# Optimization experiments

Measured on AMD Instinct MI355X. Metric: run time of the kernel, lower is better.

Reference implementation:

```python
import jax, jax.numpy as jnp
import numpy as np

R = 16
ALPHA = 16.0
SCALING = ALPHA / R  # = 1.0


def setup_inputs() -> dict:
    key = jax.random.key(0)
    k1, k2, k3 = jax.random.split(key, 3)
    x = jax.random.normal(k1, (4, 4096, 4096), dtype=jnp.float32)
    A = jax.random.normal(k2, (4096, R), dtype=jnp.float32)
    B = jax.random.normal(k3, (R, 4096), dtype=jnp.float32)
    return {"x": x, "A": A, "B": B}


def reference(x, A, B):
    # Faithful to torch: W_delta = A @ B * scaling; out = x @ W_delta
    # (dropout_p=0.0 so dropout is a no-op)
    W_delta = (A @ B) * SCALING  # [in, out]
    return jnp.matmul(x, W_delta)  # [b, s, out]
```

## Files before the change

kernel.cpp:

```cpp
#include <hip/hip_runtime.h>


constexpr int RANK = 16;
constexpr int K = 4096;
constexpr int N = 4096;
constexpr int M = 4 * 4096;
constexpr int KC = 512;
constexpr int NCHUNK = K / KC;

__global__ __launch_bounds__(512) void lora_fused(const float* __restrict__ x,
                                                  const float* __restrict__ A,
                                                  const float* __restrict__ B,
                                                  float* __restrict__ out) {
  const int tid = threadIdx.x;
  const int lane = tid & 63;
  const int w = tid >> 6;
  const int rg = w & 3;
  const int jg = w >> 2;
  const int rbase = blockIdx.x * 16;
  const int r0 = rbase + rg * 4;
  const int m = (lane >> 2) & 3;

  __shared__ float4 As[KC * 4];
  __shared__ float Ts[16][RANK];

  const float4* __restrict__ A4 = reinterpret_cast<const float4*>(A);

  float vals[32];
#pragma unroll
  for (int i = 0; i < 32; ++i) vals[i] = 0.0f;

  for (int c = 0; c < NCHUNK; ++c) {
    __syncthreads();
#pragma unroll
    for (int q = 0; q < 4; ++q) {
      const int n = q * 512 + tid;
      const int k = n >> 2;
      const int s = n & 3;
      const int p = s ^ ((k >> 2) & 3);
      As[k * 4 + p] = A4[(size_t)c * 2048 + n];
    }
    __syncthreads();

#pragma unroll
    for (int kbi = 0; kbi < 8; ++kbi) {
      const int kl = kbi * 64 + lane;
      const size_t kg = (size_t)c * KC + kl;

      float xv[4];
#pragma unroll
      for (int r = 0; r < 4; ++r) xv[r] = x[(size_t)(r0 + r) * K + kg];

      float4 a[2];
#pragma unroll
      for (int ss = 0; ss < 2; ++ss)
        a[ss] = As[kl * 4 + ((2 * jg + ss) ^ m)];

#pragma unroll
      for (int r = 0; r < 4; ++r) {
#pragma unroll
        for (int ss = 0; ss < 2; ++ss) {
          vals[r * 8 + ss * 4 + 0] = fmaf(xv[r], a[ss].x, vals[r * 8 + ss * 4 + 0]);
          vals[r * 8 + ss * 4 + 1] = fmaf(xv[r], a[ss].y, vals[r * 8 + ss * 4 + 1]);
          vals[r * 8 + ss * 4 + 2] = fmaf(xv[r], a[ss].z, vals[r * 8 + ss * 4 + 2]);
          vals[r * 8 + ss * 4 + 3] = fmaf(xv[r], a[ss].w, vals[r * 8 + ss * 4 + 3]);
        }
      }
    }
  }

#define FOLD(AH, LB)                                           \
  {                                                            \
    const bool hi = (lane & (LB)) != 0;                        \
    _Pragma("unroll")                                          \
    for (int i = 0; i < (AH); ++i) {                           \
      const float send = hi ? vals[i] : vals[i + (AH)];        \
      const float keep = hi ? vals[i + (AH)] : vals[i];        \
      vals[i] = keep + __shfl_xor(send, (LB), 64);             \
    }                                                          \
  }
  FOLD(16, 32)
  FOLD(8, 16)
  FOLD(4, 8)
  FOLD(2, 4)
  FOLD(1, 2)
#undef FOLD
  vals[0] += __shfl_xor(vals[0], 1, 64);

  if (!(lane & 1)) {
    const int e = lane >> 1;
    Ts[rg * 4 + (e >> 3)][jg * 8 + (e & 7)] = vals[0];
  }
  __syncthreads();

  const float2* __restrict__ B2 = reinterpret_cast<const float2*>(B);
  float2* __restrict__ out2 = reinterpret_cast<float2*>(out);

#pragma unroll 1
  for (int cc = 0; cc < 4; ++cc) {
    const int col = w * 512 + cc * 128 + lane * 2;

    float2 b[16];
#pragma unroll
    for (int j = 0; j < RANK; ++j) b[j] = B2[((size_t)j * N + col) >> 1];

#pragma unroll 1
    for (int r = 0; r < 16; ++r) {
      const float4* __restrict__ tr4 =
          reinterpret_cast<const float4*>(&Ts[r][0]);
      const float4 t0 = tr4[0];
      const float4 t1 = tr4[1];
      const float4 t2 = tr4[2];
      const float4 t3 = tr4[3];
      const float tsv[16] = {t0.x, t0.y, t0.z, t0.w, t1.x, t1.y, t1.z, t1.w,
                             t2.x, t2.y, t2.z, t2.w, t3.x, t3.y, t3.z, t3.w};

      float2 acc;
      acc.x = acc.y = 0.0f;
#pragma unroll
      for (int j = 0; j < RANK; ++j) {
        acc.x = fmaf(tsv[j], b[j].x, acc.x);
        acc.y = fmaf(tsv[j], b[j].y, acc.y);
      }
      out2[((size_t)(rbase + r) * N + col) >> 1] = acc;
    }
  }
}

extern "C" void kernel_launch(void* const* d_in, const int* in_sizes, int n_in,
                              void* d_out, int out_size, void* d_ws, size_t ws_size,
                              hipStream_t stream) {
  const float* x = (const float*)d_in[0];
  const float* A = (const float*)d_in[1];
  const float* B = (const float*)d_in[2];
  float* out = (float*)d_out;
  (void)d_ws; (void)ws_size;

  lora_fused<<<M / 16, 512, 0, stream>>>(x, A, B, out);
}
```

Before: 138.6 us.

## Process two row tiles per block, overlapping first tile's output with second's reduction

Each block now handles 32 rows in two halves of 16. While it computes x@A for the second half, it interleaves the B-projection and output stores for the first half into the chunk loop. The point is to overlap the write-heavy output phase with the read-heavy x streaming, and to use float4 B loads and out stores. The trade-off is half as many blocks, which lowers parallelism over the 256 CUs and adds register pressure and extra global B loads inside the hot loop.

```diff
diff --git a/kernel.cpp b/kernel.cpp
--- a/kernel.cpp
+++ b/kernel.cpp
@@ -7,6 +7,8 @@
 constexpr int M = 4 * 4096;
 constexpr int KC = 512;
 constexpr int NCHUNK = K / KC;
+constexpr int ROWST = 16;
+constexpr int ROWSB = 32;
 
 __global__ __launch_bounds__(512) void lora_fused(const float* __restrict__ x,
                                                   const float* __restrict__ A,
@@ -17,97 +19,123 @@
   const int w = tid >> 6;
   const int rg = w & 3;
   const int jg = w >> 2;
-  const int rbase = blockIdx.x * 16;
-  const int r0 = rbase + rg * 4;
+  const int rbase = blockIdx.x * ROWSB;
   const int m = (lane >> 2) & 3;
 
   __shared__ float4 As[KC * 4];
-  __shared__ float Ts[16][RANK];
+  __shared__ float Ts[2][ROWST][RANK];
 
   const float4* __restrict__ A4 = reinterpret_cast<const float4*>(A);
+  const float4* __restrict__ B4 = reinterpret_cast<const float4*>(B);
+  float4* __restrict__ out4 = reinterpret_cast<float4*>(out);
 
-  float vals[32];
+  for (int half = 0; half < 2; ++half) {
+    const int r0 = rbase + half * ROWST + rg * 4;
+
+    float vals[32];
 #pragma unroll
-  for (int i = 0; i < 32; ++i) vals[i] = 0.0f;
+    for (int i = 0; i < 32; ++i) vals[i] = 0.0f;
 
-  for (int c = 0; c < NCHUNK; ++c) {
-    __syncthreads();
+    for (int c = 0; c < NCHUNK; ++c) {
+      __syncthreads();
 #pragma unroll
-    for (int q = 0; q < 4; ++q) {
-      const int n = q * 512 + tid;
-      const int k = n >> 2;
-      const int s = n & 3;
-      const int p = s ^ ((k >> 2) & 3);
-      As[k * 4 + p] = A4[(size_t)c * 2048 + n];
-    }
-    __syncthreads();
+      for (int q = 0; q < 4; ++q) {
+        const int n = q * 512 + tid;
+        const int k = n >> 2;
+        const int s = n & 3;
+        const int p = s ^ ((k >> 2) & 3);
+        As[k * 4 + p] = A4[(size_t)c * 2048 + n];
+      }
+      __syncthreads();
+
+      if (half == 1) {
+        const int rr0 = 2 * c, rr1 = 2 * c + 1;
+#pragma unroll 1
+        for (int cc = 0; cc < 2; ++cc) {
+          const int col = w * 512 + cc * 256 + lane * 4;
+          float4 acc0, acc1;
+          acc0.x = acc0.y = acc0.z = acc0.w = 0.0f;
+          acc1.x = acc1.y = acc1.z = acc1.w = 0.0f;
+#pragma unroll 4
+          for (int j = 0; j < RANK; ++j) {
+            const float4 bj = B4[((size_t)j * N + col) >> 2];
+            const float t0 = Ts[0][rr0][j];
+            const float t1 = Ts[0][rr1][j];
+            acc0.x = fmaf(t0, bj.x, acc0.x); acc0.y = fmaf(t0, bj.y, acc0.y);
+            acc0.z = fmaf(t0, bj.z, acc0.z); acc0.w = fmaf(t0, bj.w, acc0.w);
+            acc1.x = fmaf(t1, bj.x, acc1.x); acc1.y = fmaf(t1, bj.y, acc1.y);
+            acc1.z = fmaf(t1, bj.z, acc1.z); acc1.w = fmaf(t1, bj.w, acc1.w);
+          }
+          out4[((size_t)(rbase + rr0) * N + col) >> 2] = acc0;
+          out4[((size_t)(rbase + rr1) * N + col) >> 2] = acc1;
+        }
+      }
 
 #pragma unroll
-    for (int kbi = 0; kbi < 8; ++kbi) {
-      const int kl = kbi * 64 + lane;
-      const size_t kg = (size_t)c * KC + kl;
+      for (int kbi = 0; kbi < 8; ++kbi) {
+        const int kl = kbi * 64 + lane;
+        const size_t kg = (size_t)c * KC + kl;
 
-      float xv[4];
+        float xv[4];
 #pragma unroll
-      for (int r = 0; r < 4; ++r) xv[r] = x[(size_t)(r0 + r) * K + kg];
+        for (int r = 0; r < 4; ++r) xv[r] = x[(size_t)(r0 + r) * K + kg];
 
-      float4 a[2];
+        float4 a[2];
 #pragma unroll
-      for (int ss = 0; ss < 2; ++ss)
-        a[ss] = As[kl * 4 + ((2 * jg + ss) ^ m)];
+        for (int ss = 0; ss < 2; ++ss)
+          a[ss] = As[kl * 4 + ((2 * jg + ss) ^ m)];
 
 #pragma unroll
-      for (int r = 0; r < 4; ++r) {
+        for (int r = 0; r < 4; ++r) {
 #pragma unroll
-        for (int ss = 0; ss < 2; ++ss) {
-          vals[r * 8 + ss * 4 + 0] = fmaf(xv[r], a[ss].x, vals[r * 8 + ss * 4 + 0]);
-          vals[r * 8 + ss * 4 + 1] = fmaf(xv[r], a[ss].y, vals[r * 8 + ss * 4 + 1]);
-          vals[r * 8 + ss * 4 + 2] = fmaf(xv[r], a[ss].z, vals[r * 8 + ss * 4 + 2]);
-          vals[r * 8 + ss * 4 + 3] = fmaf(xv[r], a[ss].w, vals[r * 8 + ss * 4 + 3]);
+          for (int ss = 0; ss < 2; ++ss) {
+            vals[r * 8 + ss * 4 + 0] = fmaf(xv[r], a[ss].x, vals[r * 8 + ss * 4 + 0]);
+            vals[r * 8 + ss * 4 + 1] = fmaf(xv[r], a[ss].y, vals[r * 8 + ss * 4 + 1]);
+            vals[r * 8 + ss * 4 + 2] = fmaf(xv[r], a[ss].z, vals[r * 8 + ss * 4 + 2]);
+            vals[r * 8 + ss * 4 + 3] = fmaf(xv[r], a[ss].w, vals[r * 8 + ss * 4 + 3]);
+          }
         }
       }
     }
+
+#define FOLD(AH, LB)                                           \
+    {                                                          \
+      const bool hi = (lane & (LB)) != 0;                      \
+      _Pragma("unroll")                                        \
+      for (int i = 0; i < (AH); ++i) {                         \
+        const float send = hi ? vals[i] : vals[i + (AH)];      \
+        const float keep = hi ? vals[i + (AH)] : vals[i];      \
+        vals[i] = keep + __shfl_xor(send, (LB), 64);           \
+      }                                                        \
+    }
+    FOLD(16, 32)
+    FOLD(8, 16)
+    FOLD(4, 8)
+    FOLD(2, 4)
+    FOLD(1, 2)
+#undef FOLD
+    vals[0] += __shfl_xor(vals[0], 1, 64);
+
+    if (!(lane & 1)) {
+      const int e = lane >> 1;
+      Ts[half][rg * 4 + (e >> 3)][jg * 8 + (e & 7)] = vals[0];
+    }
   }
 
-#define FOLD(AH, LB)                                           \
-  {                                                            \
-    const bool hi = (lane & (LB)) != 0;                        \
-    _Pragma("unroll")                                          \
-    for (int i = 0; i < (AH); ++i) {                           \
-      const float send = hi ? vals[i] : vals[i + (AH)];        \
-      const float keep = hi ? vals[i + (AH)] : vals[i];        \
-      vals[i] = keep + __shfl_xor(send, (LB), 64);             \
-    }                                                          \
-  }
-  FOLD(16, 32)
-  FOLD(8, 16)
-  FOLD(4, 8)
-  FOLD(2, 4)
-  FOLD(1, 2)
-#undef FOLD
-  vals[0] += __shfl_xor(vals[0], 1, 64);
-
-  if (!(lane & 1)) {
-    const int e = lane >> 1;
-    Ts[rg * 4 + (e >> 3)][jg * 8 + (e & 7)] = vals[0];
-  }
   __syncthreads();
 
-  const float2* __restrict__ B2 = reinterpret_cast<const float2*>(B);
-  float2* __restrict__ out2 = reinterpret_cast<float2*>(out);
+#pragma unroll 1
+  for (int cc = 0; cc < 2; ++cc) {
+    const int col = w * 512 + cc * 256 + lane * 4;
+
+    float4 b[16];
+#pragma unroll
+    for (int j = 0; j < RANK; ++j) b[j] = B4[((size_t)j * N + col) >> 2];
 
 #pragma unroll 1
-  for (int cc = 0; cc < 4; ++cc) {
-    const int col = w * 512 + cc * 128 + lane * 2;
-
-    float2 b[16];
-#pragma unroll
-    for (int j = 0; j < RANK; ++j) b[j] = B2[((size_t)j * N + col) >> 1];
-
-#pragma unroll 1
-    for (int r = 0; r < 16; ++r) {
+    for (int r = 0; r < ROWST; ++r) {
       const float4* __restrict__ tr4 =
-          reinterpret_cast<const float4*>(&Ts[r][0]);
+          reinterpret_cast<const float4*>(&Ts[1][r][0]);
       const float4 t0 = tr4[0];
       const float4 t1 = tr4[1];
       const float4 t2 = tr4[2];
@@ -115,14 +143,16 @@
       const float tsv[16] = {t0.x, t0.y, t0.z, t0.w, t1.x, t1.y, t1.z, t1.w,
                              t2.x, t2.y, t2.z, t2.w, t3.x, t3.y, t3.z, t3.w};
 
-      float2 acc;
-      acc.x = acc.y = 0.0f;
+      float4 acc;
+      acc.x = acc.y = acc.z = acc.w = 0.0f;
 #pragma unroll
       for (int j = 0; j < RANK; ++j) {
         acc.x = fmaf(tsv[j], b[j].x, acc.x);
         acc.y = fmaf(tsv[j], b[j].y, acc.y);
+        acc.z = fmaf(tsv[j], b[j].z, acc.z);
+        acc.w = fmaf(tsv[j], b[j].w, acc.w);
       }
-      out2[((size_t)(rbase + r) * N + col) >> 1] = acc;
+      out4[((size_t)(rbase + ROWST + r) * N + col) >> 2] = acc;
     }
   }
 }
@@ -136,5 +166,5 @@
   float* out = (float*)d_out;
   (void)d_ws; (void)ws_size;
 
-  lora_fused<<<M / 16, 512, 0, stream>>>(x, A, B, out);
+  lora_fused<<<M / ROWSB, 512, 0, stream>>>(x, A, B, out);
 }
```

New measurement: 192.0 us. 1.39x slower.
